# Kernel tuning notes

Measured on AMD Instinct MI355X. Metric: run time of the kernel, lower is better.

## Reference

```python
import jax, jax.numpy as jnp
import numpy as np

TEMP_DIV = 13.0  # forward hard-codes attn / 13 (self.temperature is unused)


def setup_inputs() -> dict:
    key = jax.random.key(0)
    k1, k2, k3 = jax.random.split(key, 3)
    B, Lq, Lk, D = 8, 2048, 2048, 640
    q = jax.random.normal(k1, (B, Lq, D), dtype=jnp.float32)
    k = jax.random.normal(k2, (B, Lk, D), dtype=jnp.float32)
    v = jax.random.normal(k3, (B, Lk, D), dtype=jnp.float32)
    return {"q": q, "k": k, "v": v}


def _l2_scores(q, k):
    # -sum((q[:,:,None,:] - k[:,None,:,:])**2, axis=3) via the GEMM expansion
    # ||q||^2 - 2 q.k + ||k||^2  -> avoids the (B,Lq,Lk,D) intermediate.
    qq = jnp.sum(q * q, axis=-1)            # (B, Lq)
    kk = jnp.sum(k * k, axis=-1)            # (B, Lk)
    qk = jnp.einsum('bqd,bkd->bqk', q, k)   # (B, Lq, Lk)
    return -(qq[:, :, None] - 2.0 * qk + kk[:, None, :])


def reference(q, k, v):
    attn_logits = _l2_scores(q, k) / TEMP_DIV          # (B, Lq, Lk)
    log_attn = jax.nn.log_softmax(attn_logits, axis=2)
    attn = jnp.exp(log_attn)                            # softmax, shares the stable pass
    # dropout is identity in eval mode
    output = jnp.einsum('bqk,bkd->bqd', attn, v)        # bmm
    return (output, attn, log_attn)
```

## Files before the change

kernel.cpp:

```cpp
#include <hip/hip_runtime.h>


#define B_   8
#define LQ   2048
#define LK   2048
#define DD   640

typedef short s16x8 __attribute__((ext_vector_type(8)));
typedef float f32x4 __attribute__((ext_vector_type(4)));

__device__ __forceinline__ unsigned short f2bf(float x) {
    unsigned int u = __float_as_uint(x);
    unsigned int r = (u + 0x7fffu + ((u >> 16) & 1u)) >> 16;
    return (unsigned short)r;
}

__global__ __launch_bounds__(256) void cvt_norm2(const float* __restrict__ q,
                                                 const float* __restrict__ k,
                                                 unsigned short* __restrict__ q16,
                                                 unsigned short* __restrict__ k16,
                                                 float* __restrict__ qq,
                                                 float* __restrict__ kkn) {
    int row  = blockIdx.x * 4 + (threadIdx.x >> 6);
    int lane = threadIdx.x & 63;
    const float* src;
    unsigned short* dst;
    float* nrm;
    int r;
    if (row < B_ * LQ) { src = q; dst = q16; nrm = qq;  r = row; }
    else               { src = k; dst = k16; nrm = kkn; r = row - B_ * LQ; }
    const float4* s = (const float4*)(src + (size_t)r * DD);
    unsigned short* d = dst + (size_t)r * DD;
    float ss = 0.f;
    for (int t = lane; t < DD / 4; t += 64) {
        float4 x = s[t];
        ss += x.x * x.x + x.y * x.y + x.z * x.z + x.w * x.w;
        ushort4 o;
        o.x = f2bf(x.x); o.y = f2bf(x.y); o.z = f2bf(x.z); o.w = f2bf(x.w);
        *(ushort4*)(d + t * 4) = o;
    }
    #pragma unroll
    for (int o = 32; o; o >>= 1) ss += __shfl_xor(ss, o);
    if (lane == 0) nrm[r] = ss;
}

__global__ __launch_bounds__(256) void cvt_transpose_v(const float* __restrict__ v,
                                                       unsigned short* __restrict__ vt) {
    __shared__ float tile[64][65];
    int bx = blockIdx.x;
    int b  = bx / 320;
    int r  = bx % 320;
    int tj = r / 10;
    int td = r % 10;
    const float* src = v + (size_t)b * LK * DD + (size_t)tj * 64 * DD + td * 64;
    for (int e = threadIdx.x; e < 4096; e += 256) {
        int rr = e >> 6, cc = e & 63;
        tile[rr][cc] = src[(size_t)rr * DD + cc];
    }
    __syncthreads();
    unsigned short* dst = vt + (size_t)b * DD * LK + (size_t)td * 64 * LK + tj * 64;
    for (int e = threadIdx.x; e < 4096; e += 256) {
        int rr = e >> 6, cc = e & 63;
        dst[(size_t)rr * LK + cc] = f2bf(tile[cc][rr]);
    }
}

template <int LDA, int LDB, int KSZ, int NTN, int BN, int WM, int WN, bool EPI>
__global__ __launch_bounds__(512, 2) void gemm_nt256(
    const unsigned short* __restrict__ A, const unsigned short* __restrict__ Bm,
    float* __restrict__ C, size_t strideA, size_t strideB, size_t strideC, int ldc,
    const float* __restrict__ qq, const float* __restrict__ kkn) {

    constexpr int KT   = KSZ / 64;
    constexpr int RM   = 256 / WM / 16;
    constexpr int RN   = BN  / WN / 16;
    constexpr int LBLD = BN / 64;

    __shared__ unsigned short lA[2 * 2 * 256 * 32];
    __shared__ unsigned short lB[2 * 2 * BN  * 32];

    int bx = blockIdx.x;
    int tm = bx & 7;
    int i  = bx >> 3;
    int tn = i % NTN;
    int b  = i / NTN;

    const unsigned short* Ab = A  + b * strideA + (size_t)tm * 256 * LDA;
    const unsigned short* Bb = Bm + b * strideB + (size_t)tn * BN  * LDB;

    int tid  = threadIdx.x;
    int w    = tid >> 6;
    int lane = tid & 63;
    int lrow = lane & 15;
    int lk4  = lane >> 4;
    int wm   = w / WN;
    int wn   = w % WN;

    auto stage = [&](int kt, int p) {
        int k0 = kt * 64;
        #pragma unroll
        for (int s = 0; s < 4; ++s) {
            int row = ((s & 1) << 7) | (tid >> 2);
            int kh  = s >> 1;
            int ch  = tid & 3;
            int sc  = k0 + kh * 32 + ((ch ^ ((row >> 1) & 3)) << 3);
            __builtin_amdgcn_global_load_lds(
                (const __attribute__((address_space(1))) void*)(Ab + (size_t)row * LDA + sc),
                (__attribute__((address_space(3))) void*)(lA + p * 16384 + s * 4096 + w * 512),
                16, 0, 0);
        }
        #pragma unroll
        for (int s = 0; s < LBLD; ++s) {
            int o  = s * 8192 + tid * 16;
            int kh = o / (BN * 64);
            int rr = (o & (BN * 64 - 1)) >> 6;
            int ch = (o >> 4) & 3;
            int sc = k0 + kh * 32 + ((ch ^ ((rr >> 1) & 3)) << 3);
            __builtin_amdgcn_global_load_lds(
                (const __attribute__((address_space(1))) void*)(Bb + (size_t)rr * LDB + sc),
                (__attribute__((address_space(3))) void*)(lB + p * (BN * 64) + s * 4096 + w * 512),
                16, 0, 0);
        }
    };

    f32x4 acc[RM][RN] = {};

    stage(0, 0);
    stage(1, 1);

    #pragma unroll 2
    for (int t = 0; t < KT; ++t) {
        int p = t & 1;
        if constexpr (BN == 256) asm volatile("s_waitcnt vmcnt(8)" ::: "memory");
        else                     asm volatile("s_waitcnt vmcnt(6)" ::: "memory");
        __builtin_amdgcn_s_barrier();
        __builtin_amdgcn_sched_barrier(0);
        asm volatile("" ::: "memory");

        const unsigned short* pA = lA + p * 16384;
        const unsigned short* pB = lB + p * (BN * 64);

        s16x8 bf[RN][2];
        #pragma unroll
        for (int n = 0; n < RN; ++n)
            #pragma unroll
            for (int kh = 0; kh < 2; ++kh) {
                int br = wn * (RN * 16) + n * 16 + lrow;
                bf[n][kh] = *(const s16x8*)(pB + kh * (BN * 32) + br * 32 +
                                            ((lk4 ^ ((br >> 1) & 3)) << 3));
            }

        #pragma unroll
        for (int qm = 0; qm < 2; ++qm) {
            s16x8 af[RM / 2][2];
            #pragma unroll
            for (int m = 0; m < RM / 2; ++m)
                #pragma unroll
                for (int kh = 0; kh < 2; ++kh) {
                    int ar = wm * (RM * 16) + (qm * (RM / 2) + m) * 16 + lrow;
                    af[m][kh] = *(const s16x8*)(pA + kh * 8192 + ar * 32 +
                                                ((lk4 ^ ((ar >> 1) & 3)) << 3));
                }
            __builtin_amdgcn_s_setprio(1);
            #pragma unroll
            for (int kh = 0; kh < 2; ++kh)
                #pragma unroll
                for (int m = 0; m < RM / 2; ++m)
                    #pragma unroll
                    for (int n = 0; n < RN; ++n)
                        acc[qm * (RM / 2) + m][n] = __builtin_amdgcn_mfma_f32_16x16x32_bf16(
                            af[m][kh], bf[n][kh], acc[qm * (RM / 2) + m][n], 0, 0, 0);
            __builtin_amdgcn_s_setprio(0);
        }

        asm volatile("" ::: "memory");
        __builtin_amdgcn_sched_barrier(0);
        __builtin_amdgcn_s_barrier();
        int t2 = (t + 2 < KT) ? t + 2 : 0;
        stage(t2, p);
    }
    asm volatile("s_waitcnt vmcnt(0)" ::: "memory");

    float* Cb = C + b * strideC + (size_t)(tm * 256) * ldc + tn * BN;
    #pragma unroll
    for (int mi = 0; mi < RM; ++mi) {
        int rb = wm * (RM * 16) + mi * 16 + lk4 * 4;
        #pragma unroll
        for (int ni = 0; ni < RN; ++ni) {
            int col = wn * (RN * 16) + ni * 16 + lrow;
            #pragma unroll
            for (int rr = 0; rr < 4; ++rr) {
                float val = acc[mi][ni][rr];
                if constexpr (EPI)
                    val = (2.0f * val - qq[b * LQ + tm * 256 + rb + rr]
                                      - kkn[b * LK + tn * BN + col]) * (1.0f / 13.0f);
                Cb[(size_t)(rb + rr) * ldc + col] = val;
            }
        }
    }
}

__global__ __launch_bounds__(256) void softmax_fix(float* __restrict__ logits,
                                                   float* __restrict__ attn,
                                                   unsigned short* __restrict__ a16) {
    __shared__ float redm[4], reds[4];
    size_t row = blockIdx.x;
    float* Lr = logits + row * LK;
    int tid = threadIdx.x;
    float x[8];
    *(float4*)(x)     = *(const float4*)(Lr + tid * 8);
    *(float4*)(x + 4) = *(const float4*)(Lr + tid * 8 + 4);

    float m = x[0];
    #pragma unroll
    for (int i = 1; i < 8; ++i) m = fmaxf(m, x[i]);
    #pragma unroll
    for (int o = 32; o; o >>= 1) m = fmaxf(m, __shfl_xor(m, o));
    int wv = tid >> 6, ln = tid & 63;
    if (ln == 0) redm[wv] = m;
    __syncthreads();
    m = fmaxf(fmaxf(redm[0], redm[1]), fmaxf(redm[2], redm[3]));

    float e[8];
    float s = 0.f;
    #pragma unroll
    for (int i = 0; i < 8; ++i) { e[i] = __expf(x[i] - m); s += e[i]; }
    #pragma unroll
    for (int o = 32; o; o >>= 1) s += __shfl_xor(s, o);
    if (ln == 0) reds[wv] = s;
    __syncthreads();
    s = reds[0] + reds[1] + reds[2] + reds[3];

    float lse = __logf(s);
    float inv = 1.0f / s;
    float at[8], la[8];
    #pragma unroll
    for (int i = 0; i < 8; ++i) { at[i] = e[i] * inv; la[i] = x[i] - m - lse; }

    float* Ar = attn + row * LK;
    *(float4*)(Ar + tid * 8)     = *(float4*)at;
    *(float4*)(Ar + tid * 8 + 4) = *(float4*)(at + 4);
    *(float4*)(Lr + tid * 8)     = *(float4*)la;
    *(float4*)(Lr + tid * 8 + 4) = *(float4*)(la + 4);

    unsigned short h[8];
    #pragma unroll
    for (int i = 0; i < 8; ++i) h[i] = f2bf(at[i]);
    unsigned short* Hr = a16 + row * LK;
    *(ushort4*)(Hr + tid * 8)     = *(ushort4*)h;
    *(ushort4*)(Hr + tid * 8 + 4) = *(ushort4*)(h + 4);
}

extern "C" void kernel_launch(void* const* d_in, const int* in_sizes, int n_in,
                              void* d_out, int out_size, void* d_ws, size_t ws_size,
                              hipStream_t stream) {
    const float* q = (const float*)d_in[0];
    const float* k = (const float*)d_in[1];
    const float* v = (const float*)d_in[2];

    float* out   = (float*)d_out;
    float* attn  = out + (size_t)B_ * LQ * DD;
    float* logat = attn + (size_t)B_ * LQ * LK;

    unsigned short* q16  = (unsigned short*)d_ws;
    unsigned short* k16  = q16 + (size_t)B_ * LQ * DD;
    unsigned short* v16t = k16 + (size_t)B_ * LK * DD;
    unsigned short* a16  = v16t + (size_t)B_ * DD * LK;
    float* qq  = (float*)(a16 + (size_t)B_ * LQ * LK);
    float* kkn = qq + (size_t)B_ * LQ;

    cvt_norm2<<<2 * B_ * LQ / 4, 256, 0, stream>>>(q, k, q16, k16, qq, kkn);
    cvt_transpose_v<<<B_ * (LK / 64) * (DD / 64), 256, 0, stream>>>(v, v16t);

    gemm_nt256<DD, DD, DD, 8, 256, 2, 4, true><<<B_ * 8 * 8, 512, 0, stream>>>(
        q16, k16, logat,
        (size_t)LQ * DD, (size_t)LK * DD, (size_t)LQ * LK, LK, qq, kkn);

    softmax_fix<<<B_ * LQ, 256, 0, stream>>>(logat, attn, a16);

    gemm_nt256<LK, LK, LK, 5, 128, 4, 2, false><<<B_ * 8 * 5, 512, 0, stream>>>(
        a16, v16t, out,
        (size_t)LQ * LK, (size_t)DD * LK, (size_t)LQ * DD, DD, nullptr, nullptr);
}
```

Baseline: 616.2 us.

## Rework GEMM into 256x256 tiles with interleaved staging and finer barriers

Replaces the GEMM kernel with a fixed 256x256 tile version that splits each k-step into four sub-phases. Loads for the next stage are issued between the MFMA groups, with barriers around each group, in the style of an 8-phase ping-pong schedule. Row and column norms are cached in shared memory for the epilogue. The second GEMM now uses 256-wide column tiles with clamped loads and masked stores for the 640-wide output, which cuts its grid from 320 to 192 blocks. This risks more barrier overhead, lower occupancy in the PV GEMM, and wasted compute on the padded last column tile.

```diff
diff --git a/kernel.cpp b/kernel.cpp
--- a/kernel.cpp
+++ b/kernel.cpp
@@ -65,19 +65,17 @@
     }
 }
 
-template <int LDA, int LDB, int KSZ, int NTN, int BN, int WM, int WN, bool EPI>
-__global__ __launch_bounds__(512, 2) void gemm_nt256(
+template <int LDA, int LDB, int KSZ, int NTN, int BCOLS, bool EPI>
+__global__ __launch_bounds__(512, 2) void gemm8p(
     const unsigned short* __restrict__ A, const unsigned short* __restrict__ Bm,
     float* __restrict__ C, size_t strideA, size_t strideB, size_t strideC, int ldc,
     const float* __restrict__ qq, const float* __restrict__ kkn) {
 
-    constexpr int KT   = KSZ / 64;
-    constexpr int RM   = 256 / WM / 16;
-    constexpr int RN   = BN  / WN / 16;
-    constexpr int LBLD = BN / 64;
-
-    __shared__ unsigned short lA[2 * 2 * 256 * 32];
-    __shared__ unsigned short lB[2 * 2 * BN  * 32];
+    constexpr int KT = KSZ / 64;
+
+    __shared__ unsigned short lA[2 * 16384];
+    __shared__ unsigned short lB[2 * 16384];
+    __shared__ float snm[512];
 
     int bx = blockIdx.x;
     int tm = bx & 7;
@@ -86,115 +84,134 @@
     int b  = i / NTN;
 
     const unsigned short* Ab = A  + b * strideA + (size_t)tm * 256 * LDA;
-    const unsigned short* Bb = Bm + b * strideB + (size_t)tn * BN  * LDB;
+    const unsigned short* Bb = Bm + b * strideB + (size_t)tn * 256 * LDB;
 
     int tid  = threadIdx.x;
     int w    = tid >> 6;
     int lane = tid & 63;
     int lrow = lane & 15;
     int lk4  = lane >> 4;
-    int wm   = w / WN;
-    int wn   = w % WN;
-
-    auto stage = [&](int kt, int p) {
-        int k0 = kt * 64;
-        #pragma unroll
-        for (int s = 0; s < 4; ++s) {
-            int row = ((s & 1) << 7) | (tid >> 2);
-            int kh  = s >> 1;
-            int ch  = tid & 3;
-            int sc  = k0 + kh * 32 + ((ch ^ ((row >> 1) & 3)) << 3);
-            __builtin_amdgcn_global_load_lds(
-                (const __attribute__((address_space(1))) void*)(Ab + (size_t)row * LDA + sc),
-                (__attribute__((address_space(3))) void*)(lA + p * 16384 + s * 4096 + w * 512),
-                16, 0, 0);
-        }
-        #pragma unroll
-        for (int s = 0; s < LBLD; ++s) {
-            int o  = s * 8192 + tid * 16;
-            int kh = o / (BN * 64);
-            int rr = (o & (BN * 64 - 1)) >> 6;
-            int ch = (o >> 4) & 3;
-            int sc = k0 + kh * 32 + ((ch ^ ((rr >> 1) & 3)) << 3);
-            __builtin_amdgcn_global_load_lds(
-                (const __attribute__((address_space(1))) void*)(Bb + (size_t)rr * LDB + sc),
-                (__attribute__((address_space(3))) void*)(lB + p * (BN * 64) + s * 4096 + w * 512),
-                16, 0, 0);
-        }
+    int wm   = w >> 2;
+    int wn   = w & 3;
+
+    int bmax = BCOLS - tn * 256; if (bmax > 256) bmax = 256;
+
+    if constexpr (EPI) {
+        snm[tid] = (tid < 256) ? qq[b * LQ + tm * 256 + tid]
+                               : kkn[b * LK + tn * 256 + (tid - 256)];
+    }
+    asm volatile("" ::: "memory");
+
+    auto stage_chunk = [&](const unsigned short* Gb, int ldg, int rmax,
+                           unsigned short* Lb, int kt, int s) {
+        int row = ((s & 1) << 7) | (tid >> 2);
+        int kh  = s >> 1;
+        int ch  = tid & 3;
+        int gr  = row < rmax ? row : rmax - 1;
+        int sc  = kt * 64 + kh * 32 + ((ch ^ ((row >> 1) & 3)) << 3);
+        __builtin_amdgcn_global_load_lds(
+            (const __attribute__((address_space(1))) void*)(Gb + (size_t)gr * ldg + sc),
+            (__attribute__((address_space(3))) void*)(Lb + s * 4096 + w * 512),
+            16, 0, 0);
     };
 
-    f32x4 acc[RM][RN] = {};
-
-    stage(0, 0);
-    stage(1, 1);
-
-    #pragma unroll 2
-    for (int t = 0; t < KT; ++t) {
-        int p = t & 1;
-        if constexpr (BN == 256) asm volatile("s_waitcnt vmcnt(8)" ::: "memory");
-        else                     asm volatile("s_waitcnt vmcnt(6)" ::: "memory");
-        __builtin_amdgcn_s_barrier();
+    #pragma unroll
+    for (int s = 0; s < 4; ++s) stage_chunk(Ab, LDA, 256,  lA,         0, s);
+    #pragma unroll
+    for (int s = 0; s < 4; ++s) stage_chunk(Bb, LDB, bmax, lB,         0, s);
+    #pragma unroll
+    for (int s = 0; s < 4; ++s) stage_chunk(Ab, LDA, 256,  lA + 16384, 1, s);
+    #pragma unroll
+    for (int s = 0; s < 4; ++s) stage_chunk(Bb, LDB, bmax, lB + 16384, 1, s);
+
+    f32x4 acc[8][4] = {};
+
+    auto bar = [&]() {
         __builtin_amdgcn_sched_barrier(0);
         asm volatile("" ::: "memory");
-
+        __builtin_amdgcn_s_barrier();
+        asm volatile("" ::: "memory");
+        __builtin_amdgcn_sched_barrier(0);
+    };
+
+    auto run_iter = [&](int t, bool st) {
+        int p = t & 1;
         const unsigned short* pA = lA + p * 16384;
-        const unsigned short* pB = lB + p * (BN * 64);
-
-        s16x8 bf[RN][2];
+        const unsigned short* pB = lB + p * 16384;
+        unsigned short* sA = lA + p * 16384;
+        unsigned short* sB = lB + p * 16384;
+        int t2 = t + 2;
+        s16x8 bf[4][2];
         #pragma unroll
-        for (int n = 0; n < RN; ++n)
+        for (int j = 0; j < 4; ++j) {
+            if (j == 0) {
+                #pragma unroll
+                for (int n = 0; n < 4; ++n)
+                    #pragma unroll
+                    for (int kh = 0; kh < 2; ++kh) {
+                        int br = wn * 64 + n * 16 + lrow;
+                        bf[n][kh] = *(const s16x8*)(pB + kh * 8192 + br * 32 +
+                                                    ((lk4 ^ ((br >> 1) & 3)) << 3));
+                    }
+            }
+            s16x8 af[2][2];
             #pragma unroll
-            for (int kh = 0; kh < 2; ++kh) {
-                int br = wn * (RN * 16) + n * 16 + lrow;
-                bf[n][kh] = *(const s16x8*)(pB + kh * (BN * 32) + br * 32 +
-                                            ((lk4 ^ ((br >> 1) & 3)) << 3));
-            }
-
-        #pragma unroll
-        for (int qm = 0; qm < 2; ++qm) {
-            s16x8 af[RM / 2][2];
-            #pragma unroll
-            for (int m = 0; m < RM / 2; ++m)
+            for (int m = 0; m < 2; ++m)
                 #pragma unroll
                 for (int kh = 0; kh < 2; ++kh) {
-                    int ar = wm * (RM * 16) + (qm * (RM / 2) + m) * 16 + lrow;
+                    int ar = wm * 128 + (j * 2 + m) * 16 + lrow;
                     af[m][kh] = *(const s16x8*)(pA + kh * 8192 + ar * 32 +
                                                 ((lk4 ^ ((ar >> 1) & 3)) << 3));
                 }
+            if (st) {
+                if (j == 1) { stage_chunk(Bb, LDB, bmax, sB, t2, 0);
+                              stage_chunk(Bb, LDB, bmax, sB, t2, 1); }
+                if (j == 2) { stage_chunk(Bb, LDB, bmax, sB, t2, 2);
+                              stage_chunk(Bb, LDB, bmax, sB, t2, 3); }
+            }
+            bar();
             __builtin_amdgcn_s_setprio(1);
             #pragma unroll
             for (int kh = 0; kh < 2; ++kh)
                 #pragma unroll
-                for (int m = 0; m < RM / 2; ++m)
+                for (int m = 0; m < 2; ++m)
                     #pragma unroll
-                    for (int n = 0; n < RN; ++n)
-                        acc[qm * (RM / 2) + m][n] = __builtin_amdgcn_mfma_f32_16x16x32_bf16(
-                            af[m][kh], bf[n][kh], acc[qm * (RM / 2) + m][n], 0, 0, 0);
+                    for (int n = 0; n < 4; ++n)
+                        acc[j * 2 + m][n] = __builtin_amdgcn_mfma_f32_16x16x32_bf16(
+                            af[m][kh], bf[n][kh], acc[j * 2 + m][n], 0, 0, 0);
             __builtin_amdgcn_s_setprio(0);
+            bar();
         }
-
-        asm volatile("" ::: "memory");
-        __builtin_amdgcn_sched_barrier(0);
-        __builtin_amdgcn_s_barrier();
-        int t2 = (t + 2 < KT) ? t + 2 : 0;
-        stage(t2, p);
+        if (st) {
+            #pragma unroll
+            for (int s = 0; s < 4; ++s) stage_chunk(Ab, LDA, 256, sA, t2, s);
+        }
+    };
+
+    for (int t = 0; t < KT - 1; ++t) {
+        asm volatile("s_waitcnt vmcnt(8)" ::: "memory");
+        bar();
+        run_iter(t, t + 2 < KT);
     }
     asm volatile("s_waitcnt vmcnt(0)" ::: "memory");
-
-    float* Cb = C + b * strideC + (size_t)(tm * 256) * ldc + tn * BN;
-    #pragma unroll
-    for (int mi = 0; mi < RM; ++mi) {
-        int rb = wm * (RM * 16) + mi * 16 + lk4 * 4;
+    bar();
+    run_iter(KT - 1, false);
+
+    float* Cb = C + b * strideC + (size_t)(tm * 256) * ldc + tn * 256;
+    #pragma unroll
+    for (int mi = 0; mi < 8; ++mi) {
+        int rb = wm * 128 + mi * 16 + lk4 * 4;
         #pragma unroll
-        for (int ni = 0; ni < RN; ++ni) {
-            int col = wn * (RN * 16) + ni * 16 + lrow;
-            #pragma unroll
-            for (int rr = 0; rr < 4; ++rr) {
-                float val = acc[mi][ni][rr];
-                if constexpr (EPI)
-                    val = (2.0f * val - qq[b * LQ + tm * 256 + rb + rr]
-                                      - kkn[b * LK + tn * BN + col]) * (1.0f / 13.0f);
-                Cb[(size_t)(rb + rr) * ldc + col] = val;
+        for (int ni = 0; ni < 4; ++ni) {
+            int col = wn * 64 + ni * 16 + lrow;
+            if (col < bmax) {
+                #pragma unroll
+                for (int rr = 0; rr < 4; ++rr) {
+                    float val = acc[mi][ni][rr];
+                    if constexpr (EPI)
+                        val = (2.0f * val - snm[rb + rr] - snm[256 + col]) * (1.0f / 13.0f);
+                    Cb[(size_t)(rb + rr) * ldc + col] = val;
+                }
             }
         }
     }
@@ -272,13 +289,13 @@
     cvt_norm2<<<2 * B_ * LQ / 4, 256, 0, stream>>>(q, k, q16, k16, qq, kkn);
     cvt_transpose_v<<<B_ * (LK / 64) * (DD / 64), 256, 0, stream>>>(v, v16t);
 
-    gemm_nt256<DD, DD, DD, 8, 256, 2, 4, true><<<B_ * 8 * 8, 512, 0, stream>>>(
+    gemm8p<DD, DD, DD, 8, LK, true><<<B_ * 8 * 8, 512, 0, stream>>>(
         q16, k16, logat,
         (size_t)LQ * DD, (size_t)LK * DD, (size_t)LQ * LK, LK, qq, kkn);
 
     softmax_fix<<<B_ * LQ, 256, 0, stream>>>(logat, attn, a16);
 
-    gemm_nt256<LK, LK, LK, 5, 128, 4, 2, false><<<B_ * 8 * 5, 512, 0, stream>>>(
+    gemm8p<LK, LK, LK, 3, DD, false><<<B_ * 3 * 8, 512, 0, stream>>>(
         a16, v16t, out,
         (size_t)LQ * LK, (size_t)DD * LK, (size_t)LQ * DD, DD, nullptr, nullptr);
 }
```

Measured after the change: 611.0 us. About the same (-0.8%).
